# Kernel tuning notes

Hardware: AMD Instinct MI355X
Metric: run time of the kernel (lower is better)

## Reference

```python
import jax, jax.numpy as jnp
import numpy as np

B, SQ, SKV, D = 4, 4096, 4096, 64

def setup_inputs() -> dict:
    key = jax.random.key(0)
    kq, kk, kv = jax.random.split(key, 3)
    return {
        "q": jax.random.normal(kq, (B, SQ, D), dtype=jnp.float32),
        "k": jax.random.normal(kk, (B, SKV, D), dtype=jnp.float32),
        "v": jax.random.normal(kv, (B, SKV, D), dtype=jnp.float32),
        "inv_scale_factor": 8,
        "is_training": 0,
    }

def reference(q, k, v, inv_scale_factor, is_training):
    # qk = q @ k^T, divided by inv_scale_factor, softmax over keys
    scores = jnp.einsum("bqd,bkd->bqk", q, k) / inv_scale_factor  # [B,SQ,SKV]
    attn = jax.nn.softmax(scores, axis=-1)
    # dropout is deterministic identity (eval mode, is_training=0)
    out = jnp.einsum("bqk,bkd->bqd", attn, v)  # [B,SQ,D]
    # should_apply_residual before loop
    out = out + q
    # 3-iteration chain: residual add + normalization add (+2q), dropout (identity),
    # sigmoid, clamp(0,1)
    for _ in range(3):
        out = out + 2.0 * q
        out = jax.nn.sigmoid(out)
        out = jnp.clip(out, 0.0, 1.0)
    return out
```

## Files before the change

### kernel.cpp

```cpp
#include <hip/hip_runtime.h>

#define SQd 4096
#define SKVd 4096
#define DDIM 64
#define BK 32
#define NG 8
#define NTILES (SKVd / BK)
#define NCHUNK (NTILES / 2)
#define TPG (NTILES / NG)
#define CPG (TPG / 2)
#define KWS_BYTES ((size_t)4 * NTILES * 2048)
#define BROWS 32

typedef float floatx4  __attribute__((ext_vector_type(4)));
typedef float floatx16 __attribute__((ext_vector_type(16)));
typedef int   intx8    __attribute__((ext_vector_type(8)));

template <bool HI>
__device__ inline int pk2(float a, float b, int old) {
    return __builtin_amdgcn_cvt_pk_fp8_f32(a, b, old, HI);
}

__device__ inline intx8 mk8(int4 a, int4 b) {
    intx8 r;
    r[0] = a.x; r[1] = a.y; r[2] = a.z; r[3] = a.w;
    r[4] = b.x; r[5] = b.y; r[6] = b.z; r[7] = b.w;
    return r;
}

struct CombS {
    float Ored[BROWS][4][68];
    float Lred[BROWS][NG];
};

__global__ __launch_bounds__(256)
void prepack_kernel(const float* __restrict__ k, const float* __restrict__ v,
                    char* __restrict__ ws)
{
    __shared__ __align__(16) float Kt[BK][68];
    __shared__ __align__(16) float Vt[BK][68];

    const int blk  = blockIdx.x;
    const int b    = blk >> 7;
    const int tile = blk & (NTILES - 1);
    const int tid  = threadIdx.x;

    const size_t base = ((size_t)b * SKVd + tile * BK) * DDIM;
    {
        const int row = tid >> 3, col = (tid & 7) * 8;
        const float4 k0 = *(const float4*)(k + base + (size_t)row * DDIM + col);
        const float4 k1 = *(const float4*)(k + base + (size_t)row * DDIM + col + 4);
        *(float4*)&Kt[row][col] = k0; *(float4*)&Kt[row][col + 4] = k1;
        const float4 v0 = *(const float4*)(v + base + (size_t)row * DDIM + col);
        const float4 v1 = *(const float4*)(v + base + (size_t)row * DDIM + col + 4);
        *(float4*)&Vt[row][col] = v0; *(float4*)&Vt[row][col + 4] = v1;
    }
    __syncthreads();

    const int lane = tid & 63;
    const int q4   = tid >> 6;
    const int l31  = lane & 31;
    const int u    = lane >> 5;

    {
        const float* s = &Kt[l31][u * 32 + q4 * 8];
        int w0 = pk2<false>(s[0], s[1], 0); w0 = pk2<true>(s[2], s[3], w0);
        int w1 = pk2<false>(s[4], s[5], 0); w1 = pk2<true>(s[6], s[7], w1);
        int2 o2; o2.x = w0; o2.y = w1;
        *(int2*)(ws + (size_t)(b * NTILES + tile) * 2048 + lane * 32 + q4 * 8) = o2;
    }
    {
        const int h  = q4 >> 1;
        const int rh = (q4 & 1) * 8;
        float p[8];
        #pragma unroll
        for (int i = 0; i < 8; ++i) {
            const int r   = rh + i;
            const int key = (r & 3) + 8 * (r >> 2) + 4 * u;
            p[i] = Vt[key][h * 32 + l31];
        }
        int w0 = pk2<false>(p[0], p[1], 0); w0 = pk2<true>(p[2], p[3], w0);
        int w1 = pk2<false>(p[4], p[5], 0); w1 = pk2<true>(p[6], p[7], w1);
        int2 o2; o2.x = w0; o2.y = w1;
        const size_t voff = KWS_BYTES
            + ((size_t)(b * NCHUNK + (tile >> 1)) * 2 + h) * 2048
            + lane * 32 + (tile & 1) * 16 + rh;
        *(int2*)(ws + voff) = o2;
    }
}

__global__ __launch_bounds__(512, 4)
void fattn_kernel(const float* __restrict__ q, const int* __restrict__ isf_p,
                  const char* __restrict__ kws, const char* __restrict__ vws,
                  float* __restrict__ out)
{
    __shared__ CombS C;

    const int tid  = threadIdx.x;
    const int g    = tid >> 6;
    const int lane = tid & 63;
    const int l31  = lane & 31;
    const int u    = lane >> 5;

    const int bidx  = blockIdx.x;
    const int b     = bidx >> 7;
    const int qbase = (bidx & 127) * BROWS;

    const float scale = 1.44269504088896340736f / (float)(*isf_p);
    const float SINIT = -4.0f * 1.44269504088896340736f;

    intx8 qf;
    {
        const float* qp = q + ((size_t)b * SQd + qbase + l31) * DDIM + u * 32;
        #pragma unroll
        for (int d = 0; d < 8; ++d) {
            const float4 a = *(const float4*)(qp + 4 * d);
            int w = pk2<false>(a.x * scale, a.y * scale, 0);
            w     = pk2<true >(a.z * scale, a.w * scale, w);
            qf[d] = w;
        }
    }

    const char* kg = kws + (size_t)(b * NTILES + g * TPG) * 2048 + lane * 32;
    const char* vg = vws + (size_t)(b * NCHUNK + g * CPG) * 4096 + lane * 32;
    const int cph  = bidx & (CPG - 1);

    floatx16 sinit16, o0, o1;
    #pragma unroll
    for (int i = 0; i < 16; ++i) { sinit16[i] = SINIT; o0[i] = 0.f; o1[i] = 0.f; }
    float l_acc = 0.f;

    #pragma unroll 1
    for (int c = 0; c < CPG; ++c) {
        const size_t off = (size_t)((c + cph) & (CPG - 1)) * 4096;
        const int4 ka0 = *(const int4*)(kg + off);
        const int4 ka1 = *(const int4*)(kg + off + 16);
        const int4 kb0 = *(const int4*)(kg + off + 2048);
        const int4 kb1 = *(const int4*)(kg + off + 2064);

        intx8 pa;
        floatx16 s = __builtin_amdgcn_mfma_scale_f32_32x32x64_f8f6f4(
            mk8(ka0, ka1), qf, sinit16, 0, 0, 0, 0x7F7F7F7F, 0, 0x7F7F7F7F);

        const int4 va0 = *(const int4*)(vg + off);
        const int4 va1 = *(const int4*)(vg + off + 16);
        const int4 vb0 = *(const int4*)(vg + off + 2048);
        const int4 vb1 = *(const int4*)(vg + off + 2064);

        {
            #pragma unroll
            for (int r = 0; r < 16; ++r) s[r] = __builtin_amdgcn_exp2f(s[r]);
            l_acc += ((((s[0] + s[1]) + (s[2] + s[3])) + ((s[4] + s[5]) + (s[6] + s[7])))
                   + (((s[8] + s[9]) + (s[10] + s[11])) + ((s[12] + s[13]) + (s[14] + s[15]))));
            #pragma unroll
            for (int d2 = 0; d2 < 4; ++d2) {
                int w = pk2<false>(s[4 * d2], s[4 * d2 + 1], 0);
                pa[d2] = pk2<true>(s[4 * d2 + 2], s[4 * d2 + 3], w);
            }
        }
        {
            floatx16 s2 = __builtin_amdgcn_mfma_scale_f32_32x32x64_f8f6f4(
                mk8(kb0, kb1), qf, sinit16, 0, 0, 0, 0x7F7F7F7F, 0, 0x7F7F7F7F);
            #pragma unroll
            for (int r = 0; r < 16; ++r) s2[r] = __builtin_amdgcn_exp2f(s2[r]);
            l_acc += ((((s2[0] + s2[1]) + (s2[2] + s2[3])) + ((s2[4] + s2[5]) + (s2[6] + s2[7])))
                   + (((s2[8] + s2[9]) + (s2[10] + s2[11])) + ((s2[12] + s2[13]) + (s2[14] + s2[15]))));
            #pragma unroll
            for (int d2 = 0; d2 < 4; ++d2) {
                int w = pk2<false>(s2[4 * d2], s2[4 * d2 + 1], 0);
                pa[4 + d2] = pk2<true>(s2[4 * d2 + 2], s2[4 * d2 + 3], w);
            }
        }
        o0 = __builtin_amdgcn_mfma_scale_f32_32x32x64_f8f6f4(
            pa, mk8(va0, va1), o0, 0, 0, 0, 0x7F7F7F7F, 0, 0x7F7F7F7F);
        o1 = __builtin_amdgcn_mfma_scale_f32_32x32x64_f8f6f4(
            pa, mk8(vb0, vb1), o1, 0, 0, 0, 0x7F7F7F7F, 0, 0x7F7F7F7F);
    }

    l_acc += __shfl_xor(l_acc, 32);
    if (u == 0) C.Lred[l31][g] = l_acc;

    if (g < 4) {
        #pragma unroll
        for (int r = 0; r < 16; ++r) {
            const int row = (r & 3) + 8 * (r >> 2) + 4 * u;
            C.Ored[row][g][l31]      = o0[r];
            C.Ored[row][g][32 + l31] = o1[r];
        }
    }
    __syncthreads();
    if (g >= 4) {
        #pragma unroll
        for (int r = 0; r < 16; ++r) {
            const int row = (r & 3) + 8 * (r >> 2) + 4 * u;
            C.Ored[row][g - 4][l31]      += o0[r];
            C.Ored[row][g - 4][32 + l31] += o1[r];
        }
    }
    __syncthreads();

    {
        const int row = tid >> 4;
        const int d4  = (tid & 15) * 4;
        float l = 0.0f;
        #pragma unroll
        for (int gg = 0; gg < NG; ++gg) l += C.Lred[row][gg];
        const float rl = 1.0f / l;
        float xs[4] = {0.f, 0.f, 0.f, 0.f};
        #pragma unroll
        for (int s = 0; s < 4; ++s) {
            const float4 t4 = *(const float4*)&C.Ored[row][s][d4];
            xs[0] += t4.x; xs[1] += t4.y; xs[2] += t4.z; xs[3] += t4.w;
        }
        const size_t idx = ((size_t)b * SQd + qbase + row) * DDIM + d4;
        const float4 q4v = *(const float4*)(q + idx);
        const float qs[4] = {q4v.x, q4v.y, q4v.z, q4v.w};
        #pragma unroll
        for (int c = 0; c < 4; ++c) {
            float x = xs[c] * rl + qs[c];
            #pragma unroll
            for (int itc = 0; itc < 3; ++itc) {
                x = x + 2.0f * qs[c];
                x = 1.0f / (1.0f + __expf(-x));
                x = fminf(fmaxf(x, 0.0f), 1.0f);
            }
            xs[c] = x;
        }
        const float4 r4 = {xs[0], xs[1], xs[2], xs[3]};
        *(float4*)(out + idx) = r4;
    }
}

extern "C" void kernel_launch(void* const* d_in, const int* in_sizes, int n_in,
                              void* d_out, int out_size, void* d_ws, size_t ws_size,
                              hipStream_t stream) {
    const float* q = (const float*)d_in[0];
    const float* k = (const float*)d_in[1];
    const float* v = (const float*)d_in[2];
    const int* isf = (const int*)d_in[3];
    float* out = (float*)d_out;
    char* ws = (char*)d_ws;

    prepack_kernel<<<dim3(4 * NTILES), dim3(256), 0, stream>>>(k, v, ws);

    const int nblocks = 4 * (SQd / BROWS);
    fattn_kernel<<<dim3(nblocks), dim3(512), 0, stream>>>(
        q, isf, ws, ws + KWS_BYTES, out);
}
```

Before: 89.41 us.

## Software-pipeline QK MFMAs one chunk ahead of softmax and PV

Restructures the main loop so that the QK^T MFMAs for the next chunk are issued before the exp2/pack work on the current chunk's scores, with K loads prefetched two chunks ahead. The loop is manually unrolled by two with ping-pong score registers. The SINIT offset moves from the MFMA accumulator init into the exp2 argument, so the MFMA accumulator starts from zero. This is meant to hide MFMA and load latency behind VALU work, at the cost of more live registers (two extra floatx16 score buffers), which could lower occupancy. It also issues extra wrapped K loads past the last chunk.

Result: slower. 130.3 us (+45.7%).

```diff
diff --git a/kernel.cpp b/kernel.cpp
--- a/kernel.cpp
+++ b/kernel.cpp
@@ -125,56 +125,76 @@
     const char* vg = vws + (size_t)(b * NCHUNK + g * CPG) * 4096 + lane * 32;
     const int cph  = bidx & (CPG - 1);
 
-    floatx16 sinit16, o0, o1;
+    floatx16 o0, o1;
     #pragma unroll
-    for (int i = 0; i < 16; ++i) { sinit16[i] = SINIT; o0[i] = 0.f; o1[i] = 0.f; }
+    for (int i = 0; i < 16; ++i) { o0[i] = 0.f; o1[i] = 0.f; }
+    const floatx16 zc = o0;
     float l_acc = 0.f;
 
-    #pragma unroll 1
-    for (int c = 0; c < CPG; ++c) {
+    int4 ka0, ka1, kb0, kb1;
+    auto loadK = [&](int c) {
         const size_t off = (size_t)((c + cph) & (CPG - 1)) * 4096;
-        const int4 ka0 = *(const int4*)(kg + off);
-        const int4 ka1 = *(const int4*)(kg + off + 16);
-        const int4 kb0 = *(const int4*)(kg + off + 2048);
-        const int4 kb1 = *(const int4*)(kg + off + 2064);
+        ka0 = *(const int4*)(kg + off);        ka1 = *(const int4*)(kg + off + 16);
+        kb0 = *(const int4*)(kg + off + 2048); kb1 = *(const int4*)(kg + off + 2064);
+    };
+
+    loadK(0);
+    floatx16 sA = __builtin_amdgcn_mfma_scale_f32_32x32x64_f8f6f4(
+        mk8(ka0, ka1), qf, zc, 0, 0, 0, 0x7F7F7F7F, 0, 0x7F7F7F7F);
+    floatx16 sB = __builtin_amdgcn_mfma_scale_f32_32x32x64_f8f6f4(
+        mk8(kb0, kb1), qf, zc, 0, 0, 0, 0x7F7F7F7F, 0, 0x7F7F7F7F);
+    loadK(1);
+    floatx16 sA2, sB2;
+
+    auto step = [&](floatx16& sc_a, floatx16& sc_b,
+                    floatx16& sn_a, floatx16& sn_b, int c) {
+        sn_a = __builtin_amdgcn_mfma_scale_f32_32x32x64_f8f6f4(
+            mk8(ka0, ka1), qf, zc, 0, 0, 0, 0x7F7F7F7F, 0, 0x7F7F7F7F);
+        sn_b = __builtin_amdgcn_mfma_scale_f32_32x32x64_f8f6f4(
+            mk8(kb0, kb1), qf, zc, 0, 0, 0, 0x7F7F7F7F, 0, 0x7F7F7F7F);
+
+        const size_t offc = (size_t)((c + cph) & (CPG - 1)) * 4096;
+        const int4 va0 = *(const int4*)(vg + offc);
+        const int4 va1 = *(const int4*)(vg + offc + 16);
+        const int4 vb0 = *(const int4*)(vg + offc + 2048);
+        const int4 vb1 = *(const int4*)(vg + offc + 2064);
 
         intx8 pa;
-        floatx16 s = __builtin_amdgcn_mfma_scale_f32_32x32x64_f8f6f4(
-            mk8(ka0, ka1), qf, sinit16, 0, 0, 0, 0x7F7F7F7F, 0, 0x7F7F7F7F);
-
-        const int4 va0 = *(const int4*)(vg + off);
-        const int4 va1 = *(const int4*)(vg + off + 16);
-        const int4 vb0 = *(const int4*)(vg + off + 2048);
-        const int4 vb1 = *(const int4*)(vg + off + 2064);
-
-        {
-            #pragma unroll
-            for (int r = 0; r < 16; ++r) s[r] = __builtin_amdgcn_exp2f(s[r]);
-            l_acc += ((((s[0] + s[1]) + (s[2] + s[3])) + ((s[4] + s[5]) + (s[6] + s[7])))
-                   + (((s[8] + s[9]) + (s[10] + s[11])) + ((s[12] + s[13]) + (s[14] + s[15]))));
-            #pragma unroll
-            for (int d2 = 0; d2 < 4; ++d2) {
-                int w = pk2<false>(s[4 * d2], s[4 * d2 + 1], 0);
-                pa[d2] = pk2<true>(s[4 * d2 + 2], s[4 * d2 + 3], w);
-            }
-        }
-        {
-            floatx16 s2 = __builtin_amdgcn_mfma_scale_f32_32x32x64_f8f6f4(
-                mk8(kb0, kb1), qf, sinit16, 0, 0, 0, 0x7F7F7F7F, 0, 0x7F7F7F7F);
-            #pragma unroll
-            for (int r = 0; r < 16; ++r) s2[r] = __builtin_amdgcn_exp2f(s2[r]);
-            l_acc += ((((s2[0] + s2[1]) + (s2[2] + s2[3])) + ((s2[4] + s2[5]) + (s2[6] + s2[7])))
-                   + (((s2[8] + s2[9]) + (s2[10] + s2[11])) + ((s2[12] + s2[13]) + (s2[14] + s2[15]))));
-            #pragma unroll
-            for (int d2 = 0; d2 < 4; ++d2) {
-                int w = pk2<false>(s2[4 * d2], s2[4 * d2 + 1], 0);
-                pa[4 + d2] = pk2<true>(s2[4 * d2 + 2], s2[4 * d2 + 3], w);
-            }
-        }
+        #pragma unroll
+        for (int r = 0; r < 16; ++r) sc_a[r] = __builtin_amdgcn_exp2f(sc_a[r] + SINIT);
+        l_acc += ((((sc_a[0] + sc_a[1]) + (sc_a[2] + sc_a[3]))
+                 + ((sc_a[4] + sc_a[5]) + (sc_a[6] + sc_a[7])))
+                + (((sc_a[8] + sc_a[9]) + (sc_a[10] + sc_a[11]))
+                 + ((sc_a[12] + sc_a[13]) + (sc_a[14] + sc_a[15]))));
+        #pragma unroll
+        for (int d2 = 0; d2 < 4; ++d2) {
+            int w = pk2<false>(sc_a[4 * d2], sc_a[4 * d2 + 1], 0);
+            pa[d2] = pk2<true>(sc_a[4 * d2 + 2], sc_a[4 * d2 + 3], w);
+        }
+        #pragma unroll
+        for (int r = 0; r < 16; ++r) sc_b[r] = __builtin_amdgcn_exp2f(sc_b[r] + SINIT);
+        l_acc += ((((sc_b[0] + sc_b[1]) + (sc_b[2] + sc_b[3]))
+                 + ((sc_b[4] + sc_b[5]) + (sc_b[6] + sc_b[7])))
+                + (((sc_b[8] + sc_b[9]) + (sc_b[10] + sc_b[11]))
+                 + ((sc_b[12] + sc_b[13]) + (sc_b[14] + sc_b[15]))));
+        #pragma unroll
+        for (int d2 = 0; d2 < 4; ++d2) {
+            int w = pk2<false>(sc_b[4 * d2], sc_b[4 * d2 + 1], 0);
+            pa[4 + d2] = pk2<true>(sc_b[4 * d2 + 2], sc_b[4 * d2 + 3], w);
+        }
+
+        loadK(c + 2);
+
         o0 = __builtin_amdgcn_mfma_scale_f32_32x32x64_f8f6f4(
             pa, mk8(va0, va1), o0, 0, 0, 0, 0x7F7F7F7F, 0, 0x7F7F7F7F);
         o1 = __builtin_amdgcn_mfma_scale_f32_32x32x64_f8f6f4(
             pa, mk8(vb0, vb1), o1, 0, 0, 0, 0x7F7F7F7F, 0, 0x7F7F7F7F);
+    };
+
+    #pragma unroll 1
+    for (int c = 0; c < CPG; c += 2) {
+        step(sA, sB, sA2, sB2, c);
+        step(sA2, sB2, sA, sB, c + 1);
     }
 
     l_acc += __shfl_xor(l_acc, 32);
```
